# Optimization experiments

Measured on AMD Instinct MI355X. Metric: run time of the kernel, lower is better.

The kernel has to match this reference:

```python
import jax, jax.numpy as jnp
import numpy as np

B = 32768          # batch size (positions)
PIECES = 32        # max active features per position
NNZ = B * PIECES
FT_OUT = 512
NFEAT = 768        # 64 squares * 6 piece types * 2 colors


def setup_inputs() -> dict:
    key = jax.random.key(0)
    k1, k2, k3, k4, k5, k6 = jax.random.split(key, 6)
    rows = jnp.repeat(jnp.arange(B, dtype=jnp.int64), PIECES)  # batch index per nnz
    stm_cols = jax.random.randint(k1, (NNZ,), 0, NFEAT, dtype=jnp.int64)
    nstm_cols = jax.random.randint(k2, (NNZ,), 0, NFEAT, dtype=jnp.int64)
    stm_indices = jnp.stack([rows, stm_cols], axis=0)   # [2, NNZ]
    nstm_indices = jnp.stack([rows, nstm_cols], axis=0)  # [2, NNZ]
    values = jnp.ones((NNZ,), dtype=jnp.float32)
    ft_w = jax.random.normal(k3, (FT_OUT, NFEAT), dtype=jnp.float32) * 0.05
    ft_b = jax.random.normal(k4, (FT_OUT,), dtype=jnp.float32) * 0.05
    out_w = jax.random.normal(k5, (1, 2 * FT_OUT), dtype=jnp.float32) * 0.05
    out_b = jax.random.normal(k6, (1,), dtype=jnp.float32) * 0.05
    return {
        "stm_indices": stm_indices,
        "nstm_indices": nstm_indices,
        "values": values,
        "size": B,
        "ft_w": ft_w,
        "ft_b": ft_b,
        "out_w": out_w,
        "out_b": out_b,
    }


def reference(stm_indices, nstm_indices, values, size, ft_w, ft_b, out_w, out_b):
    # sparse_coo_tensor(...).to_dense(): scatter-add values into dense [size, 768]
    board_stm = jnp.zeros((size, NFEAT), dtype=values.dtype).at[
        stm_indices[0], stm_indices[1]].add(values)
    board_nstm = jnp.zeros((size, NFEAT), dtype=values.dtype).at[
        nstm_indices[0], nstm_indices[1]].add(values)
    # shared feature transformer Linear(768, ft_out)
    stm_ft = board_stm @ ft_w.T + ft_b    # [B, FT_OUT]
    nstm_ft = board_nstm @ ft_w.T + ft_b  # [B, FT_OUT]
    hidden = jnp.clip(jnp.concatenate([stm_ft, nstm_ft], axis=1), 0.0, 1.0)
    return jax.nn.sigmoid(hidden @ out_w.T + out_b)  # [B, 1]
```

## Files before the change

kernel.cpp:

```cpp
#include <hip/hip_runtime.h>

#define BATCH  32768
#define PIECES 32
#define NNZ    (BATCH * PIECES)
#define FT_OUT 512
#define NFEAT  768
#define WSCALE 400.0f

#define POS_PER_BLOCK 32
#define NTHREADS 512
#define NBLOCKS (BATCH / POS_PER_BLOCK)
#define ROW_PITCH 784
#define SIDE_BYTES (POS_PER_BLOCK * ROW_PITCH)
#define PACC_OFF (2 * SIDE_BYTES)
#define LDS_TOTAL (PACC_OFF + 128)
#define SC_PITCH 33

typedef int v4i  __attribute__((ext_vector_type(4)));
typedef int v16i __attribute__((ext_vector_type(16)));

__global__ __launch_bounds__(256) void pack_w_i8(
    const float* __restrict__ ft_w, unsigned char* __restrict__ bpk)
{
    int gid = blockIdx.x * 256 + threadIdx.x;
    int t   = gid / 1536;
    int rem = gid - t * 1536;
    int s   = rem >> 6;
    int l   = rem & 63;
    int g   = l >> 5, ln = l & 31;
    int n   = t * 32 + ln;
    const float* src = ft_w + n * NFEAT + s * 32 + g * 16;
    unsigned ud[4];
    #pragma unroll
    for (int d = 0; d < 4; ++d) {
        unsigned u = 0;
        #pragma unroll
        for (int b = 0; b < 4; ++b) {
            float q = rintf(src[4 * d + b] * WSCALE);
            q = fminf(fmaxf(q, -127.0f), 127.0f);
            u |= ((unsigned)(int)q & 0xffu) << (8 * b);
        }
        ud[d] = u;
    }
    *(uint4*)(bpk + gid * 16) = make_uint4(ud[0], ud[1], ud[2], ud[3]);
}

__global__ __launch_bounds__(NTHREADS, 4) void nn_mfma(
    const int*   __restrict__ stm_idx,
    const int*   __restrict__ nstm_idx,
    const float* __restrict__ values,
    const unsigned char* __restrict__ bpk,
    const float* __restrict__ ft_b,
    const float* __restrict__ out_w,
    const float* __restrict__ out_b,
    float*       __restrict__ out)
{
    extern __shared__ __align__(16) unsigned char lds[];
    unsigned* ldsw = (unsigned*)lds;
    float*    scf  = (float*)lds;
    float*    pacc = (float*)(lds + PACC_OFF);

    const int tid  = threadIdx.x;
    const int pos0 = blockIdx.x * POS_PER_BLOCK;

    int colv[4], vqv[4];
    #pragma unroll
    for (int it = 0; it < 4; ++it) {
        int i    = tid + it * NTHREADS;
        int side = i >> 10;
        int r    = i & 1023;
        int nnz  = pos0 * PIECES + r;
        colv[it] = side ? nstm_idx[NNZ + nnz] : stm_idx[NNZ + nnz];
        vqv[it]  = (int)rintf(values[nnz]);
    }

    for (int i = tid; i < LDS_TOTAL / 16; i += NTHREADS)
        ((uint4*)lds)[i] = make_uint4(0u, 0u, 0u, 0u);
    __syncthreads();

    #pragma unroll
    for (int it = 0; it < 4; ++it) {
        int i    = tid + it * NTHREADS;
        int side = i >> 10;
        int pos  = (i & 1023) >> 5;
        int dw   = (side * SIDE_BYTES + pos * ROW_PITCH) >> 2;
        atomicAdd(&ldsw[dw + (colv[it] >> 2)],
                  (unsigned)vqv[it] << (8 * (colv[it] & 3)));
    }
    __syncthreads();

    const int lane = tid & 63, wv = tid >> 6;
    const int ln = lane & 31, g = lane >> 5;
    const float inv_s = 1.0f / WSCALE;

    v16i acc[2][2];
    #pragma unroll
    for (int q = 0; q < 2; ++q)
        #pragma unroll
        for (int sd = 0; sd < 2; ++sd)
            #pragma unroll
            for (int e = 0; e < 16; ++e) acc[q][sd][e] = 0;

    const unsigned char* a0p = lds + ln * ROW_PITCH + g * 16;
    const unsigned char* a1p = a0p + SIDE_BYTES;
    const unsigned char* bp0 = bpk + ((wv * 2 + 0) * 24) * 1024 + lane * 16;
    const unsigned char* bp1 = bpk + ((wv * 2 + 1) * 24) * 1024 + lane * 16;

    #pragma unroll 4
    for (int ks = 0; ks < 24; ++ks) {
        uint4 aw0 = *(const uint4*)(a0p + ks * 32);
        uint4 aw1 = *(const uint4*)(a1p + ks * 32);
        uint4 bw0 = *(const uint4*)(bp0 + ks * 1024);
        uint4 bw1 = *(const uint4*)(bp1 + ks * 1024);
        v4i af0 = __builtin_bit_cast(v4i, aw0);
        v4i af1 = __builtin_bit_cast(v4i, aw1);
        v4i bf0 = __builtin_bit_cast(v4i, bw0);
        v4i bf1 = __builtin_bit_cast(v4i, bw1);
        acc[0][0] = __builtin_amdgcn_mfma_i32_32x32x32_i8(af0, bf0, acc[0][0], 0, 0, 0);
        acc[0][1] = __builtin_amdgcn_mfma_i32_32x32x32_i8(af1, bf0, acc[0][1], 0, 0, 0);
        acc[1][0] = __builtin_amdgcn_mfma_i32_32x32x32_i8(af0, bf1, acc[1][0], 0, 0, 0);
        acc[1][1] = __builtin_amdgcn_mfma_i32_32x32x32_i8(af1, bf1, acc[1][1], 0, 0, 0);
    }

    float pp[16];
    #pragma unroll
    for (int r = 0; r < 16; ++r) pp[r] = 0.f;

    #pragma unroll
    for (int q = 0; q < 2; ++q) {
        int   n    = (wv * 2 + q) * 32 + ln;
        float bias = ft_b[n];
        float ow0  = out_w[n];
        float ow1  = out_w[FT_OUT + n];
        #pragma unroll
        for (int r = 0; r < 16; ++r) {
            float h0 = fminf(fmaxf((float)acc[q][0][r] * inv_s + bias, 0.f), 1.f);
            float h1 = fminf(fmaxf((float)acc[q][1][r] * inv_s + bias, 0.f), 1.f);
            pp[r] += h0 * ow0 + h1 * ow1;
        }
    }

    __syncthreads();
    {
        int base = wv * (32 * SC_PITCH) + ln * SC_PITCH;
        #pragma unroll
        for (int r = 0; r < 16; ++r) {
            int m = (r & 3) + 8 * (r >> 2) + 4 * g;
            scf[base + m] = pp[r];
        }
    }
    __syncthreads();
    {
        int m = tid & 31, j = tid >> 5;
        float s = 0.f;
        #pragma unroll
        for (int i = 0; i < 16; ++i) {
            int p   = i * 16 + j;
            int wvp = p >> 5, lnp = p & 31;
            s += scf[wvp * (32 * SC_PITCH) + lnp * SC_PITCH + m];
        }
        atomicAdd(&pacc[m], s);
    }
    __syncthreads();

    if (tid < POS_PER_BLOCK) {
        float p = pacc[tid] + out_b[0];
        out[pos0 + tid] = 1.0f / (1.0f + expf(-p));
    }
}

extern "C" void kernel_launch(void* const* d_in, const int* in_sizes, int n_in,
                              void* d_out, int out_size, void* d_ws, size_t ws_size,
                              hipStream_t stream)
{
    const int*   stm    = (const int*)  d_in[0];
    const int*   nstm   = (const int*)  d_in[1];
    const float* values = (const float*)d_in[2];
    const float* ft_w   = (const float*)d_in[4];
    const float* ft_b   = (const float*)d_in[5];
    const float* out_w  = (const float*)d_in[6];
    const float* out_b  = (const float*)d_in[7];

    unsigned char* bpk = (unsigned char*)d_ws;

    (void)hipFuncSetAttribute((const void*)nn_mfma,
                              hipFuncAttributeMaxDynamicSharedMemorySize,
                              LDS_TOTAL);

    pack_w_i8<<<dim3(96), dim3(256), 0, stream>>>(ft_w, bpk);
    nn_mfma<<<dim3(NBLOCKS), dim3(NTHREADS), LDS_TOTAL, stream>>>(
        stm, nstm, values, bpk, ft_b, out_w, out_b, (float*)d_out);
}
```

Baseline: 105.4 us.

## Process 64 positions per block to reuse packed weight loads across two row tiles

```diff
diff --git a/kernel.cpp b/kernel.cpp
--- a/kernel.cpp
+++ b/kernel.cpp
@@ -7,14 +7,15 @@
 #define NFEAT  768
 #define WSCALE 400.0f
 
-#define POS_PER_BLOCK 32
+#define POS_PER_BLOCK 64
 #define NTHREADS 512
 #define NBLOCKS (BATCH / POS_PER_BLOCK)
 #define ROW_PITCH 784
 #define SIDE_BYTES (POS_PER_BLOCK * ROW_PITCH)
+#define RT_BYTES   (32 * ROW_PITCH)
 #define PACC_OFF (2 * SIDE_BYTES)
-#define LDS_TOTAL (PACC_OFF + 128)
-#define SC_PITCH 33
+#define LDS_TOTAL (PACC_OFF + 256)
+#define SC_PITCH 68
 
 typedef int v4i  __attribute__((ext_vector_type(4)));
 typedef int v16i __attribute__((ext_vector_type(16)));
@@ -45,7 +46,7 @@
     *(uint4*)(bpk + gid * 16) = make_uint4(ud[0], ud[1], ud[2], ud[3]);
 }
 
-__global__ __launch_bounds__(NTHREADS, 4) void nn_mfma(
+__global__ __launch_bounds__(NTHREADS, 2) void nn_mfma(
     const int*   __restrict__ stm_idx,
     const int*   __restrict__ nstm_idx,
     const float* __restrict__ values,
@@ -63,15 +64,15 @@
     const int tid  = threadIdx.x;
     const int pos0 = blockIdx.x * POS_PER_BLOCK;
 
-    int colv[4], vqv[4];
-    #pragma unroll
-    for (int it = 0; it < 4; ++it) {
+    int colv[8], vqv[4];
+    #pragma unroll
+    for (int it = 0; it < 8; ++it) {
         int i    = tid + it * NTHREADS;
-        int side = i >> 10;
-        int r    = i & 1023;
+        int side = i >> 11;
+        int r    = i & 2047;
         int nnz  = pos0 * PIECES + r;
         colv[it] = side ? nstm_idx[NNZ + nnz] : stm_idx[NNZ + nnz];
-        vqv[it]  = (int)rintf(values[nnz]);
+        if (it < 4) vqv[it] = (int)rintf(values[nnz]);
     }
 
     for (int i = tid; i < LDS_TOTAL / 16; i += NTHREADS)
@@ -79,13 +80,13 @@
     __syncthreads();
 
     #pragma unroll
-    for (int it = 0; it < 4; ++it) {
+    for (int it = 0; it < 8; ++it) {
         int i    = tid + it * NTHREADS;
-        int side = i >> 10;
-        int pos  = (i & 1023) >> 5;
+        int side = i >> 11;
+        int pos  = (i & 2047) >> 5;
         int dw   = (side * SIDE_BYTES + pos * ROW_PITCH) >> 2;
         atomicAdd(&ldsw[dw + (colv[it] >> 2)],
-                  (unsigned)vqv[it] << (8 * (colv[it] & 3)));
+                  (unsigned)vqv[it & 3] << (8 * (colv[it] & 3)));
     }
     __syncthreads();
 
@@ -93,38 +94,49 @@
     const int ln = lane & 31, g = lane >> 5;
     const float inv_s = 1.0f / WSCALE;
 
-    v16i acc[2][2];
+    v16i acc[2][2][2];
     #pragma unroll
     for (int q = 0; q < 2; ++q)
         #pragma unroll
-        for (int sd = 0; sd < 2; ++sd)
+        for (int rt = 0; rt < 2; ++rt)
             #pragma unroll
-            for (int e = 0; e < 16; ++e) acc[q][sd][e] = 0;
-
-    const unsigned char* a0p = lds + ln * ROW_PITCH + g * 16;
-    const unsigned char* a1p = a0p + SIDE_BYTES;
+            for (int sd = 0; sd < 2; ++sd)
+                #pragma unroll
+                for (int e = 0; e < 16; ++e) acc[q][rt][sd][e] = 0;
+
+    const unsigned char* a00 = lds + ln * ROW_PITCH + g * 16;
     const unsigned char* bp0 = bpk + ((wv * 2 + 0) * 24) * 1024 + lane * 16;
     const unsigned char* bp1 = bpk + ((wv * 2 + 1) * 24) * 1024 + lane * 16;
 
     #pragma unroll 4
     for (int ks = 0; ks < 24; ++ks) {
-        uint4 aw0 = *(const uint4*)(a0p + ks * 32);
-        uint4 aw1 = *(const uint4*)(a1p + ks * 32);
-        uint4 bw0 = *(const uint4*)(bp0 + ks * 1024);
-        uint4 bw1 = *(const uint4*)(bp1 + ks * 1024);
-        v4i af0 = __builtin_bit_cast(v4i, aw0);
-        v4i af1 = __builtin_bit_cast(v4i, aw1);
-        v4i bf0 = __builtin_bit_cast(v4i, bw0);
-        v4i bf1 = __builtin_bit_cast(v4i, bw1);
-        acc[0][0] = __builtin_amdgcn_mfma_i32_32x32x32_i8(af0, bf0, acc[0][0], 0, 0, 0);
-        acc[0][1] = __builtin_amdgcn_mfma_i32_32x32x32_i8(af1, bf0, acc[0][1], 0, 0, 0);
-        acc[1][0] = __builtin_amdgcn_mfma_i32_32x32x32_i8(af0, bf1, acc[1][0], 0, 0, 0);
-        acc[1][1] = __builtin_amdgcn_mfma_i32_32x32x32_i8(af1, bf1, acc[1][1], 0, 0, 0);
-    }
-
-    float pp[16];
-    #pragma unroll
-    for (int r = 0; r < 16; ++r) pp[r] = 0.f;
+        uint4 w00 = *(const uint4*)(a00 + ks * 32);
+        uint4 w01 = *(const uint4*)(a00 + SIDE_BYTES + ks * 32);
+        uint4 w10 = *(const uint4*)(a00 + RT_BYTES + ks * 32);
+        uint4 w11 = *(const uint4*)(a00 + SIDE_BYTES + RT_BYTES + ks * 32);
+        uint4 u0  = *(const uint4*)(bp0 + ks * 1024);
+        uint4 u1  = *(const uint4*)(bp1 + ks * 1024);
+        v4i a_00 = __builtin_bit_cast(v4i, w00);
+        v4i a_01 = __builtin_bit_cast(v4i, w01);
+        v4i a_10 = __builtin_bit_cast(v4i, w10);
+        v4i a_11 = __builtin_bit_cast(v4i, w11);
+        v4i b0   = __builtin_bit_cast(v4i, u0);
+        v4i b1   = __builtin_bit_cast(v4i, u1);
+        acc[0][0][0] = __builtin_amdgcn_mfma_i32_32x32x32_i8(a_00, b0, acc[0][0][0], 0, 0, 0);
+        acc[0][0][1] = __builtin_amdgcn_mfma_i32_32x32x32_i8(a_01, b0, acc[0][0][1], 0, 0, 0);
+        acc[0][1][0] = __builtin_amdgcn_mfma_i32_32x32x32_i8(a_10, b0, acc[0][1][0], 0, 0, 0);
+        acc[0][1][1] = __builtin_amdgcn_mfma_i32_32x32x32_i8(a_11, b0, acc[0][1][1], 0, 0, 0);
+        acc[1][0][0] = __builtin_amdgcn_mfma_i32_32x32x32_i8(a_00, b1, acc[1][0][0], 0, 0, 0);
+        acc[1][0][1] = __builtin_amdgcn_mfma_i32_32x32x32_i8(a_01, b1, acc[1][0][1], 0, 0, 0);
+        acc[1][1][0] = __builtin_amdgcn_mfma_i32_32x32x32_i8(a_10, b1, acc[1][1][0], 0, 0, 0);
+        acc[1][1][1] = __builtin_amdgcn_mfma_i32_32x32x32_i8(a_11, b1, acc[1][1][1], 0, 0, 0);
+    }
+
+    float pp[2][16];
+    #pragma unroll
+    for (int rt = 0; rt < 2; ++rt)
+        #pragma unroll
+        for (int r = 0; r < 16; ++r) pp[rt][r] = 0.f;
 
     #pragma unroll
     for (int q = 0; q < 2; ++q) {
@@ -133,31 +145,36 @@
         float ow0  = out_w[n];
         float ow1  = out_w[FT_OUT + n];
         #pragma unroll
-        for (int r = 0; r < 16; ++r) {
-            float h0 = fminf(fmaxf((float)acc[q][0][r] * inv_s + bias, 0.f), 1.f);
-            float h1 = fminf(fmaxf((float)acc[q][1][r] * inv_s + bias, 0.f), 1.f);
-            pp[r] += h0 * ow0 + h1 * ow1;
+        for (int rt = 0; rt < 2; ++rt) {
+            #pragma unroll
+            for (int r = 0; r < 16; ++r) {
+                float h0 = fminf(fmaxf((float)acc[q][rt][0][r] * inv_s + bias, 0.f), 1.f);
+                float h1 = fminf(fmaxf((float)acc[q][rt][1][r] * inv_s + bias, 0.f), 1.f);
+                pp[rt][r] += h0 * ow0 + h1 * ow1;
+            }
         }
     }
 
     __syncthreads();
     {
-        int base = wv * (32 * SC_PITCH) + ln * SC_PITCH;
-        #pragma unroll
-        for (int r = 0; r < 16; ++r) {
-            int m = (r & 3) + 8 * (r >> 2) + 4 * g;
-            scf[base + m] = pp[r];
+        int base = (wv * 32 + ln) * SC_PITCH;
+        #pragma unroll
+        for (int rt = 0; rt < 2; ++rt) {
+            #pragma unroll
+            for (int r = 0; r < 16; ++r) {
+                int m = rt * 32 + (r & 3) + 8 * (r >> 2) + 4 * g;
+                scf[base + m] = pp[rt][r];
+            }
         }
     }
     __syncthreads();
     {
-        int m = tid & 31, j = tid >> 5;
+        int m = tid & 63, j = tid >> 6;
         float s = 0.f;
         #pragma unroll
-        for (int i = 0; i < 16; ++i) {
-            int p   = i * 16 + j;
-            int wvp = p >> 5, lnp = p & 31;
-            s += scf[wvp * (32 * SC_PITCH) + lnp * SC_PITCH + m];
+        for (int i = 0; i < 32; ++i) {
+            int p = i * 8 + j;
+            s += scf[p * SC_PITCH + m];
         }
         atomicAdd(&pacc[m], s);
     }
```

Result: no change. 103.4 us (-1.9%).
